# Kernel tuning notes

Measured on AMD Instinct MI355X. Metric: run time of the kernel, lower is better.

## Reference

```python
import jax, jax.numpy as jnp
import numpy as np

HEAD_COUNT = 6  # module scales by head_count**-0.5, not head_size
SCALE = HEAD_COUNT ** (-0.5)


def setup_inputs() -> dict:
    key = jax.random.key(0)
    kx, kq, kk, kv = jax.random.split(key, 4)
    B, T, C, H = 512, 128, 384, 64
    x = jax.random.normal(kx, (B, T, C), dtype=jnp.float32)
    init = (1.0 / np.sqrt(C)).astype(np.float32)
    Wq = jax.random.normal(kq, (C, H), dtype=jnp.float32) * init
    Wk = jax.random.normal(kk, (C, H), dtype=jnp.float32) * init
    Wv = jax.random.normal(kv, (C, H), dtype=jnp.float32) * init
    return {"x": x, "Wq": Wq, "Wk": Wk, "Wv": Wv}


def reference(x, Wq, Wk, Wv):
    # x: [B, T, C]; Wq/Wk/Wv: [C, H]
    q = jnp.einsum('btc,ch->bth', x, Wq)
    k = jnp.einsum('btc,ch->bth', x, Wk)
    v = jnp.einsum('btc,ch->bth', x, Wv)
    # scores: [B, T, T], scaled by head_count**-0.5 (faithful to source)
    scores = jnp.einsum('bth,bsh->bts', q, k) * SCALE
    T = x.shape[1]
    causal = jnp.tril(jnp.ones((T, T), dtype=bool))
    scores = jnp.where(causal, scores, -jnp.inf)
    weights = jax.nn.softmax(scores, axis=-1)
    # dropout omitted (eval mode / identity for reference baseline)
    return jnp.einsum('bts,bsh->bth', weights, v)
```

## Files before the change

### kernel.cpp

```cpp
#include <hip/hip_runtime.h>
#include <hip/hip_bf16.h>


#define B_ 512
#define T_ 128
#define C_ 384
#define H_ 64

typedef __bf16 bf16;
typedef __attribute__((ext_vector_type(8))) __bf16 bf16x8;
typedef __attribute__((ext_vector_type(4))) __bf16 bf16x4;
typedef __attribute__((ext_vector_type(4))) float f32x4;


__launch_bounds__(256, 2)
__global__ void head_fused(const float* __restrict__ x,
                           const float* __restrict__ Wq,
                           const float* __restrict__ Wk,
                           const float* __restrict__ Wv,
                           float* __restrict__ out)
{
    __shared__ bf16 lds[32256];
    bf16* Ws  = lds;
    bf16* Qs  = lds + 7680;
    bf16* Ks  = lds + 15872;
    bf16* Vts = lds + 24064;
    bf16* Ps  = lds + 7680;

    const int tid  = threadIdx.x;
    const int w    = tid >> 6;
    const int lane = tid & 63;
    const int lm   = lane & 15;
    const int quad = lane >> 4;
    const int b    = blockIdx.x;

    const float* xb = x + (size_t)b * (T_ * C_);

    f32x4 acc[2][12];
#pragma unroll
    for (int i = 0; i < 2; ++i)
#pragma unroll
        for (int t = 0; t < 12; ++t) acc[i][t] = (f32x4){0.f, 0.f, 0.f, 0.f};

    for (int kc = 0; kc < 12; ++kc) {
#pragma unroll
        for (int it = 0; it < 6; ++it) {
            int u   = tid + it * 256;
            int h   = u & 63;
            int rem = u >> 6;
            int j   = rem >> 3;
            int k4  = rem & 7;
            const float* Wp = (j == 0) ? Wq : (j == 1) ? Wk : Wv;
            const float* g  = Wp + (kc * 32 + k4 * 4) * H_ + h;
            float f0 = g[0], f1 = g[64], f2 = g[128], f3 = g[192];
            bf16x4 v4 = {(bf16)f0, (bf16)f1, (bf16)f2, (bf16)f3};
            *(bf16x4*)&Ws[(j * 64 + h) * 40 + k4 * 4] = v4;
        }
        __syncthreads();

        bf16x8 afr[2];
#pragma unroll
        for (int i = 0; i < 2; ++i) {
            const float4* xp =
                (const float4*)(xb + (32 * w + 16 * i + lm) * C_ + kc * 32 + quad * 8);
            float4 p0 = xp[0], p1 = xp[1];
            afr[i] = (bf16x8){(bf16)p0.x, (bf16)p0.y, (bf16)p0.z, (bf16)p0.w,
                              (bf16)p1.x, (bf16)p1.y, (bf16)p1.z, (bf16)p1.w};
        }
#pragma unroll
        for (int tn = 0; tn < 12; ++tn) {
            bf16x8 bfr = *(const bf16x8*)&Ws[(16 * tn + lm) * 40 + quad * 8];
            acc[0][tn] = __builtin_amdgcn_mfma_f32_16x16x32_bf16(afr[0], bfr, acc[0][tn], 0, 0, 0);
            acc[1][tn] = __builtin_amdgcn_mfma_f32_16x16x32_bf16(afr[1], bfr, acc[1][tn], 0, 0, 0);
        }
        __syncthreads();
    }

#pragma unroll
    for (int i = 0; i < 2; ++i) {
#pragma unroll
        for (int tn = 0; tn < 12; ++tn) {
            int gn = 16 * tn + lm;
            int j = gn >> 6, h = gn & 63;
            int m0 = 32 * w + 16 * i + quad * 4;
            if (j == 2) {
                bf16x4 v4 = {(bf16)acc[i][tn][0], (bf16)acc[i][tn][1],
                             (bf16)acc[i][tn][2], (bf16)acc[i][tn][3]};
                int pc = (m0 & 7) | ((((m0 >> 3) ^ (h & 15)) & 15) << 3);
                *(bf16x4*)&Vts[h * 128 + pc] = v4;
            } else {
                bf16* dst = (j == 0) ? Qs : Ks;
#pragma unroll
                for (int r = 0; r < 4; ++r) {
                    int m = m0 + r;
                    int pc = (h & 7) | ((((h >> 3) ^ (m & 7)) & 7) << 3);
                    dst[m * 64 + pc] = (bf16)acc[i][tn][r];
                }
            }
        }
    }
    __syncthreads();

    const float SCALE = 0.40824829046386307f;
    const int tmg0 = w, tmg1 = 7 - w;

    f32x4 sacc[2][8];
#pragma unroll
    for (int i = 0; i < 2; ++i)
#pragma unroll
        for (int t = 0; t < 8; ++t) sacc[i][t] = (f32x4){0.f, 0.f, 0.f, 0.f};

#pragma unroll
    for (int i = 0; i < 2; ++i) {
        const int tm = i ? tmg1 : tmg0;
        const int mrow = 16 * tm + lm;
        bf16x8 qa[2];
#pragma unroll
        for (int ks = 0; ks < 2; ++ks) {
            int phys = ((ks * 4 + quad) ^ (mrow & 7)) & 7;
            qa[ks] = *(const bf16x8*)&Qs[mrow * 64 + phys * 8];
        }
#pragma unroll
        for (int tn = 0; tn < 8; ++tn) {
            if (tn <= tm) {
                int nrow = 16 * tn + lm;
#pragma unroll
                for (int ks = 0; ks < 2; ++ks) {
                    int phys = ((ks * 4 + quad) ^ (nrow & 7)) & 7;
                    bf16x8 kb = *(const bf16x8*)&Ks[nrow * 64 + phys * 8];
                    sacc[i][tn] =
                        __builtin_amdgcn_mfma_f32_16x16x32_bf16(qa[ks], kb, sacc[i][tn], 0, 0, 0);
                }
            }
        }
    }

#pragma unroll
    for (int i = 0; i < 2; ++i) {
        const int tm = i ? tmg1 : tmg0;
#pragma unroll
        for (int r = 0; r < 4; ++r) {
            int m = 16 * tm + quad * 4 + r;
            float mx = -1e30f;
#pragma unroll
            for (int tn = 0; tn < 8; ++tn) {
                if (tn <= tm) {
                    int n = 16 * tn + lm;
                    float v = (n <= m) ? sacc[i][tn][r] * SCALE : -1e30f;
                    sacc[i][tn][r] = v;
                    mx = fmaxf(mx, v);
                }
            }
#pragma unroll
            for (int off = 1; off < 16; off <<= 1) mx = fmaxf(mx, __shfl_xor(mx, off, 16));
            float sum = 0.f;
#pragma unroll
            for (int tn = 0; tn < 8; ++tn) {
                if (tn <= tm) {
                    float e = __expf(sacc[i][tn][r] - mx);
                    sacc[i][tn][r] = e;
                    sum += e;
                }
            }
#pragma unroll
            for (int off = 1; off < 16; off <<= 1) sum += __shfl_xor(sum, off, 16);
            float inv = 1.f / sum;
#pragma unroll
            for (int tn = 0; tn < 8; ++tn) {
                if (tn <= tm) sacc[i][tn][r] *= inv;
            }
        }
    }

    __syncthreads();

#pragma unroll
    for (int i = 0; i < 2; ++i) {
        const int tm = i ? tmg1 : tmg0;
#pragma unroll
        for (int tn = 0; tn < 8; ++tn) {
            if (tn <= tm) {
                int n = 16 * tn + lm;
#pragma unroll
                for (int r = 0; r < 4; ++r) {
                    int m = 16 * tm + quad * 4 + r;
                    int pc = (n & 7) | ((((n >> 3) ^ (m & 15)) & 15) << 3);
                    Ps[m * 128 + pc] = (bf16)sacc[i][tn][r];
                }
            }
        }
        if ((tm & 1) == 0) {
            int m = 16 * tm + lm;
            int c0 = 16 * (tm + 1) + quad * 4;
            int pc = (c0 & 7) | ((((c0 >> 3) ^ (m & 15)) & 15) << 3);
            *(bf16x4*)&Ps[m * 128 + pc] =
                (bf16x4){(bf16)0.f, (bf16)0.f, (bf16)0.f, (bf16)0.f};
        }
    }

    f32x4 oacc[2][4];
#pragma unroll
    for (int i = 0; i < 2; ++i)
#pragma unroll
        for (int t = 0; t < 4; ++t) oacc[i][t] = (f32x4){0.f, 0.f, 0.f, 0.f};

#pragma unroll
    for (int i = 0; i < 2; ++i) {
        const int tm = i ? tmg1 : tmg0;
        const int mrow = 16 * tm + lm;
        const int nks = (tm + 2) >> 1;
        for (int ks = 0; ks < nks; ++ks) {
            int unit = ks * 4 + quad;
            int phys = (unit ^ (mrow & 15)) & 15;
            bf16x8 pa = *(const bf16x8*)&Ps[mrow * 128 + phys * 8];
#pragma unroll
            for (int th = 0; th < 4; ++th) {
                int hrow = 16 * th + lm;
                int ph2 = (unit ^ (hrow & 15)) & 15;
                bf16x8 vb = *(const bf16x8*)&Vts[hrow * 128 + ph2 * 8];
                oacc[i][th] =
                    __builtin_amdgcn_mfma_f32_16x16x32_bf16(pa, vb, oacc[i][th], 0, 0, 0);
            }
        }
    }

    float* ob = out + (size_t)b * (T_ * H_);
#pragma unroll
    for (int i = 0; i < 2; ++i) {
        const int tm = i ? tmg1 : tmg0;
#pragma unroll
        for (int th = 0; th < 4; ++th) {
            int h = 16 * th + lm;
#pragma unroll
            for (int r = 0; r < 4; ++r) {
                int m = 16 * tm + quad * 4 + r;
                ob[m * 64 + h] = oacc[i][th][r];
            }
        }
    }
}

extern "C" void kernel_launch(void* const* d_in, const int* in_sizes, int n_in,
                              void* d_out, int out_size, void* d_ws, size_t ws_size,
                              hipStream_t stream) {
    const float* x  = (const float*)d_in[0];
    const float* Wq = (const float*)d_in[1];
    const float* Wk = (const float*)d_in[2];
    const float* Wv = (const float*)d_in[3];
    float* o = (float*)d_out;
    head_fused<<<dim3(B_), dim3(256), 0, stream>>>(x, Wq, Wk, Wv, o);
}
```

Measured before the change: 173.6 us.

## Pre-convert weights to bf16 in a separate kernel and use 512-thread blocks

A small pre-pass kernel transposes and converts Wq/Wk/Wv to a bf16 [192x384] buffer in workspace. The main kernel then reads weight fragments straight from global/L2 instead of staging them in LDS each k-chunk, which removes the per-chunk __syncthreads pairs and shrinks LDS use. Blocks grow to 512 threads (8 waves), each owning one 16-row tile, which drops the previous balanced causal pairing of row tiles. The cost is an extra launch, more global weight traffic per block, and uneven causal work across waves.

Result: slower. 217.4 us (+25.2%).

```diff
diff --git a/kernel.cpp b/kernel.cpp
--- a/kernel.cpp
+++ b/kernel.cpp
@@ -12,20 +12,32 @@
 typedef __attribute__((ext_vector_type(4))) __bf16 bf16x4;
 typedef __attribute__((ext_vector_type(4))) float f32x4;
 
-
-__launch_bounds__(256, 2)
+__global__ void wt_conv(const float* __restrict__ Wq,
+                        const float* __restrict__ Wk,
+                        const float* __restrict__ Wv,
+                        bf16* __restrict__ Wt)
+{
+    int idx = blockIdx.x * 256 + threadIdx.x;
+    int n  = idx / 48;
+    int k0 = (idx - n * 48) * 8;
+    int j = n >> 6, h = n & 63;
+    const float* W = (j == 0) ? Wq : (j == 1) ? Wk : Wv;
+    bf16x8 v;
+#pragma unroll
+    for (int r = 0; r < 8; ++r) v[r] = (bf16)W[(k0 + r) * 64 + h];
+    *(bf16x8*)&Wt[n * 384 + k0] = v;
+}
+
+__launch_bounds__(512, 4)
 __global__ void head_fused(const float* __restrict__ x,
-                           const float* __restrict__ Wq,
-                           const float* __restrict__ Wk,
-                           const float* __restrict__ Wv,
+                           const bf16* __restrict__ Wt,
                            float* __restrict__ out)
 {
-    __shared__ bf16 lds[32256];
-    bf16* Ws  = lds;
-    bf16* Qs  = lds + 7680;
-    bf16* Ks  = lds + 15872;
-    bf16* Vts = lds + 24064;
-    bf16* Ps  = lds + 7680;
+    __shared__ bf16 lds[24576];
+    bf16* Qs  = lds;
+    bf16* Ks  = lds + 8192;
+    bf16* Vts = lds + 16384;
+    bf16* Ps  = lds;
 
     const int tid  = threadIdx.x;
     const int w    = tid >> 6;
@@ -35,207 +47,152 @@
     const int b    = blockIdx.x;
 
     const float* xb = x + (size_t)b * (T_ * C_);
-
-    f32x4 acc[2][12];
-#pragma unroll
-    for (int i = 0; i < 2; ++i)
-#pragma unroll
-        for (int t = 0; t < 12; ++t) acc[i][t] = (f32x4){0.f, 0.f, 0.f, 0.f};
-
+    const int mrow = 16 * w + lm;
+
+    f32x4 acc[12];
+#pragma unroll
+    for (int t = 0; t < 12; ++t) acc[t] = (f32x4){0.f, 0.f, 0.f, 0.f};
+
+#pragma unroll 1
     for (int kc = 0; kc < 12; ++kc) {
-#pragma unroll
-        for (int it = 0; it < 6; ++it) {
-            int u   = tid + it * 256;
-            int h   = u & 63;
-            int rem = u >> 6;
-            int j   = rem >> 3;
-            int k4  = rem & 7;
-            const float* Wp = (j == 0) ? Wq : (j == 1) ? Wk : Wv;
-            const float* g  = Wp + (kc * 32 + k4 * 4) * H_ + h;
-            float f0 = g[0], f1 = g[64], f2 = g[128], f3 = g[192];
-            bf16x4 v4 = {(bf16)f0, (bf16)f1, (bf16)f2, (bf16)f3};
-            *(bf16x4*)&Ws[(j * 64 + h) * 40 + k4 * 4] = v4;
-        }
-        __syncthreads();
-
-        bf16x8 afr[2];
-#pragma unroll
-        for (int i = 0; i < 2; ++i) {
-            const float4* xp =
-                (const float4*)(xb + (32 * w + 16 * i + lm) * C_ + kc * 32 + quad * 8);
-            float4 p0 = xp[0], p1 = xp[1];
-            afr[i] = (bf16x8){(bf16)p0.x, (bf16)p0.y, (bf16)p0.z, (bf16)p0.w,
-                              (bf16)p1.x, (bf16)p1.y, (bf16)p1.z, (bf16)p1.w};
-        }
+        const float4* xp = (const float4*)(xb + mrow * C_ + kc * 32 + quad * 8);
+        float4 p0 = xp[0], p1 = xp[1];
+        bf16x8 afr = {(bf16)p0.x, (bf16)p0.y, (bf16)p0.z, (bf16)p0.w,
+                      (bf16)p1.x, (bf16)p1.y, (bf16)p1.z, (bf16)p1.w};
 #pragma unroll
         for (int tn = 0; tn < 12; ++tn) {
-            bf16x8 bfr = *(const bf16x8*)&Ws[(16 * tn + lm) * 40 + quad * 8];
-            acc[0][tn] = __builtin_amdgcn_mfma_f32_16x16x32_bf16(afr[0], bfr, acc[0][tn], 0, 0, 0);
-            acc[1][tn] = __builtin_amdgcn_mfma_f32_16x16x32_bf16(afr[1], bfr, acc[1][tn], 0, 0, 0);
-        }
-        __syncthreads();
-    }
-
-#pragma unroll
-    for (int i = 0; i < 2; ++i) {
-#pragma unroll
-        for (int tn = 0; tn < 12; ++tn) {
-            int gn = 16 * tn + lm;
-            int j = gn >> 6, h = gn & 63;
-            int m0 = 32 * w + 16 * i + quad * 4;
-            if (j == 2) {
-                bf16x4 v4 = {(bf16)acc[i][tn][0], (bf16)acc[i][tn][1],
-                             (bf16)acc[i][tn][2], (bf16)acc[i][tn][3]};
-                int pc = (m0 & 7) | ((((m0 >> 3) ^ (h & 15)) & 15) << 3);
-                *(bf16x4*)&Vts[h * 128 + pc] = v4;
-            } else {
-                bf16* dst = (j == 0) ? Qs : Ks;
-#pragma unroll
-                for (int r = 0; r < 4; ++r) {
-                    int m = m0 + r;
-                    int pc = (h & 7) | ((((h >> 3) ^ (m & 7)) & 7) << 3);
-                    dst[m * 64 + pc] = (bf16)acc[i][tn][r];
-                }
+            bf16x8 bfr = *(const bf16x8*)&Wt[(16 * tn + lm) * 384 + kc * 32 + quad * 8];
+            acc[tn] = __builtin_amdgcn_mfma_f32_16x16x32_bf16(afr, bfr, acc[tn], 0, 0, 0);
+        }
+    }
+
+#pragma unroll
+    for (int tn = 0; tn < 12; ++tn) {
+        int h  = (16 * tn + lm) & 63;
+        int m0 = 16 * w + quad * 4;
+        if (tn >= 8) {
+            bf16x4 v4 = {(bf16)acc[tn][0], (bf16)acc[tn][1],
+                         (bf16)acc[tn][2], (bf16)acc[tn][3]};
+            int pc = (m0 & 7) | ((((m0 >> 3) ^ (h & 15)) & 15) << 3);
+            *(bf16x4*)&Vts[h * 128 + pc] = v4;
+        } else {
+            bf16* dst = (tn < 4) ? Qs : Ks;
+#pragma unroll
+            for (int r = 0; r < 4; ++r) {
+                int m = m0 + r;
+                int pc = (h & 7) | ((((h >> 3) ^ (m & 7)) & 7) << 3);
+                dst[m * 64 + pc] = (bf16)acc[tn][r];
             }
         }
     }
     __syncthreads();
 
     const float SCALE = 0.40824829046386307f;
-    const int tmg0 = w, tmg1 = 7 - w;
-
-    f32x4 sacc[2][8];
-#pragma unroll
-    for (int i = 0; i < 2; ++i)
-#pragma unroll
-        for (int t = 0; t < 8; ++t) sacc[i][t] = (f32x4){0.f, 0.f, 0.f, 0.f};
-
-#pragma unroll
-    for (int i = 0; i < 2; ++i) {
-        const int tm = i ? tmg1 : tmg0;
-        const int mrow = 16 * tm + lm;
-        bf16x8 qa[2];
-#pragma unroll
-        for (int ks = 0; ks < 2; ++ks) {
-            int phys = ((ks * 4 + quad) ^ (mrow & 7)) & 7;
-            qa[ks] = *(const bf16x8*)&Qs[mrow * 64 + phys * 8];
-        }
-#pragma unroll
-        for (int tn = 0; tn < 8; ++tn) {
-            if (tn <= tm) {
-                int nrow = 16 * tn + lm;
-#pragma unroll
-                for (int ks = 0; ks < 2; ++ks) {
-                    int phys = ((ks * 4 + quad) ^ (nrow & 7)) & 7;
-                    bf16x8 kb = *(const bf16x8*)&Ks[nrow * 64 + phys * 8];
-                    sacc[i][tn] =
-                        __builtin_amdgcn_mfma_f32_16x16x32_bf16(qa[ks], kb, sacc[i][tn], 0, 0, 0);
-                }
-            }
-        }
-    }
-
-#pragma unroll
-    for (int i = 0; i < 2; ++i) {
-        const int tm = i ? tmg1 : tmg0;
-#pragma unroll
-        for (int r = 0; r < 4; ++r) {
-            int m = 16 * tm + quad * 4 + r;
-            float mx = -1e30f;
-#pragma unroll
-            for (int tn = 0; tn < 8; ++tn) {
-                if (tn <= tm) {
-                    int n = 16 * tn + lm;
-                    float v = (n <= m) ? sacc[i][tn][r] * SCALE : -1e30f;
-                    sacc[i][tn][r] = v;
-                    mx = fmaxf(mx, v);
-                }
-            }
-#pragma unroll
-            for (int off = 1; off < 16; off <<= 1) mx = fmaxf(mx, __shfl_xor(mx, off, 16));
-            float sum = 0.f;
-#pragma unroll
-            for (int tn = 0; tn < 8; ++tn) {
-                if (tn <= tm) {
-                    float e = __expf(sacc[i][tn][r] - mx);
-                    sacc[i][tn][r] = e;
-                    sum += e;
-                }
-            }
-#pragma unroll
-            for (int off = 1; off < 16; off <<= 1) sum += __shfl_xor(sum, off, 16);
-            float inv = 1.f / sum;
-#pragma unroll
-            for (int tn = 0; tn < 8; ++tn) {
-                if (tn <= tm) sacc[i][tn][r] *= inv;
-            }
-        }
-    }
-
-    __syncthreads();
-
-#pragma unroll
-    for (int i = 0; i < 2; ++i) {
-        const int tm = i ? tmg1 : tmg0;
+    const int tm = w;
+
+    f32x4 sacc[8];
+#pragma unroll
+    for (int t = 0; t < 8; ++t) sacc[t] = (f32x4){0.f, 0.f, 0.f, 0.f};
+
+    bf16x8 qa[2];
+#pragma unroll
+    for (int ks = 0; ks < 2; ++ks) {
+        int phys = ((ks * 4 + quad) ^ (mrow & 7)) & 7;
+        qa[ks] = *(const bf16x8*)&Qs[mrow * 64 + phys * 8];
+    }
+#pragma unroll
+    for (int tn = 0; tn < 8; ++tn) {
+        if (tn <= tm) {
+            int nrow = 16 * tn + lm;
+#pragma unroll
+            for (int ks = 0; ks < 2; ++ks) {
+                int phys = ((ks * 4 + quad) ^ (nrow & 7)) & 7;
+                bf16x8 kb = *(const bf16x8*)&Ks[nrow * 64 + phys * 8];
+                sacc[tn] = __builtin_amdgcn_mfma_f32_16x16x32_bf16(qa[ks], kb, sacc[tn], 0, 0, 0);
+            }
+        }
+    }
+
+#pragma unroll
+    for (int r = 0; r < 4; ++r) {
+        int m = 16 * tm + quad * 4 + r;
+        float mx = -1e30f;
 #pragma unroll
         for (int tn = 0; tn < 8; ++tn) {
             if (tn <= tm) {
                 int n = 16 * tn + lm;
-#pragma unroll
-                for (int r = 0; r < 4; ++r) {
-                    int m = 16 * tm + quad * 4 + r;
-                    int pc = (n & 7) | ((((n >> 3) ^ (m & 15)) & 15) << 3);
-                    Ps[m * 128 + pc] = (bf16)sacc[i][tn][r];
-                }
-            }
-        }
-        if ((tm & 1) == 0) {
-            int m = 16 * tm + lm;
-            int c0 = 16 * (tm + 1) + quad * 4;
-            int pc = (c0 & 7) | ((((c0 >> 3) ^ (m & 15)) & 15) << 3);
-            *(bf16x4*)&Ps[m * 128 + pc] =
-                (bf16x4){(bf16)0.f, (bf16)0.f, (bf16)0.f, (bf16)0.f};
-        }
-    }
-
-    f32x4 oacc[2][4];
-#pragma unroll
-    for (int i = 0; i < 2; ++i)
-#pragma unroll
-        for (int t = 0; t < 4; ++t) oacc[i][t] = (f32x4){0.f, 0.f, 0.f, 0.f};
-
-#pragma unroll
-    for (int i = 0; i < 2; ++i) {
-        const int tm = i ? tmg1 : tmg0;
-        const int mrow = 16 * tm + lm;
-        const int nks = (tm + 2) >> 1;
-        for (int ks = 0; ks < nks; ++ks) {
-            int unit = ks * 4 + quad;
-            int phys = (unit ^ (mrow & 15)) & 15;
-            bf16x8 pa = *(const bf16x8*)&Ps[mrow * 128 + phys * 8];
-#pragma unroll
-            for (int th = 0; th < 4; ++th) {
-                int hrow = 16 * th + lm;
-                int ph2 = (unit ^ (hrow & 15)) & 15;
-                bf16x8 vb = *(const bf16x8*)&Vts[hrow * 128 + ph2 * 8];
-                oacc[i][th] =
-                    __builtin_amdgcn_mfma_f32_16x16x32_bf16(pa, vb, oacc[i][th], 0, 0, 0);
-            }
-        }
-    }
-
-    float* ob = out + (size_t)b * (T_ * H_);
-#pragma unroll
-    for (int i = 0; i < 2; ++i) {
-        const int tm = i ? tmg1 : tmg0;
-#pragma unroll
-        for (int th = 0; th < 4; ++th) {
-            int h = 16 * th + lm;
+                float v = (n <= m) ? sacc[tn][r] * SCALE : -1e30f;
+                sacc[tn][r] = v;
+                mx = fmaxf(mx, v);
+            }
+        }
+#pragma unroll
+        for (int off = 1; off < 16; off <<= 1) mx = fmaxf(mx, __shfl_xor(mx, off, 16));
+        float sum = 0.f;
+#pragma unroll
+        for (int tn = 0; tn < 8; ++tn) {
+            if (tn <= tm) {
+                float e = __expf(sacc[tn][r] - mx);
+                sacc[tn][r] = e;
+                sum += e;
+            }
+        }
+#pragma unroll
+        for (int off = 1; off < 16; off <<= 1) sum += __shfl_xor(sum, off, 16);
+        float inv = 1.f / sum;
+#pragma unroll
+        for (int tn = 0; tn < 8; ++tn) {
+            if (tn <= tm) sacc[tn][r] *= inv;
+        }
+    }
+
+    __syncthreads();
+
+#pragma unroll
+    for (int tn = 0; tn < 8; ++tn) {
+        if (tn <= tm) {
+            int n = 16 * tn + lm;
 #pragma unroll
             for (int r = 0; r < 4; ++r) {
                 int m = 16 * tm + quad * 4 + r;
-                ob[m * 64 + h] = oacc[i][th][r];
-            }
+                int pc = (n & 7) | ((((n >> 3) ^ (m & 15)) & 15) << 3);
+                Ps[m * 128 + pc] = (bf16)sacc[tn][r];
+            }
+        }
+    }
+    if ((tm & 1) == 0) {
+        int m = 16 * tm + lm;
+        int c0 = 16 * (tm + 1) + quad * 4;
+        int pc = (c0 & 7) | ((((c0 >> 3) ^ (m & 15)) & 15) << 3);
+        *(bf16x4*)&Ps[m * 128 + pc] = (bf16x4){(bf16)0.f, (bf16)0.f, (bf16)0.f, (bf16)0.f};
+    }
+
+    f32x4 oacc[4];
+#pragma unroll
+    for (int t = 0; t < 4; ++t) oacc[t] = (f32x4){0.f, 0.f, 0.f, 0.f};
+
+    const int nks = (tm + 2) >> 1;
+    for (int ks = 0; ks < nks; ++ks) {
+        int unit = ks * 4 + quad;
+        int phys = (unit ^ (mrow & 15)) & 15;
+        bf16x8 pa = *(const bf16x8*)&Ps[mrow * 128 + phys * 8];
+#pragma unroll
+        for (int th = 0; th < 4; ++th) {
+            int hrow = 16 * th + lm;
+            int ph2 = (unit ^ (hrow & 15)) & 15;
+            bf16x8 vb = *(const bf16x8*)&Vts[hrow * 128 + ph2 * 8];
+            oacc[th] = __builtin_amdgcn_mfma_f32_16x16x32_bf16(pa, vb, oacc[th], 0, 0, 0);
+        }
+    }
+
+    float* ob = out + (size_t)b * (T_ * H_);
+#pragma unroll
+    for (int th = 0; th < 4; ++th) {
+        int h = 16 * th + lm;
+#pragma unroll
+        for (int r = 0; r < 4; ++r) {
+            int m = 16 * tm + quad * 4 + r;
+            ob[m * 64 + h] = oacc[th][r];
         }
     }
 }
@@ -247,6 +204,8 @@
     const float* Wq = (const float*)d_in[1];
     const float* Wk = (const float*)d_in[2];
     const float* Wv = (const float*)d_in[3];
-    float* o = (float*)d_out;
-    head_fused<<<dim3(B_), dim3(256), 0, stream>>>(x, Wq, Wk, Wv, o);
+    float* o  = (float*)d_out;
+    bf16* Wt  = (bf16*)d_ws;
+    wt_conv<<<dim3(36), dim3(256), 0, stream>>>(Wq, Wk, Wv, Wt);
+    head_fused<<<dim3(B_), dim3(512), 0, stream>>>(x, Wt, o);
 }
```

## Pre-convert weights to transposed bf16 in workspace and read fragments from global

Applied to the files above, without the earlier changes.

Adds a small pre-kernel that converts Wq/Wk/Wv to a transposed bf16 matrix in the workspace. The main kernel then reads MFMA B-fragments straight from global/L2 instead of staging weights through LDS, which removes two barriers per k-chunk and shrinks LDS use. It also double-buffers the x loads one chunk ahead in registers. The costs are an extra kernel launch and repeated per-block global reads of the weights, which rely on L2 hits.

Result: slower. 191.9 us (+10.5%).

```diff
diff --git a/kernel.cpp b/kernel.cpp
--- a/kernel.cpp
+++ b/kernel.cpp
@@ -12,20 +12,32 @@
 typedef __attribute__((ext_vector_type(4))) __bf16 bf16x4;
 typedef __attribute__((ext_vector_type(4))) float f32x4;
 
+__global__ void wt_conv(const float* __restrict__ Wq,
+                        const float* __restrict__ Wk,
+                        const float* __restrict__ Wv,
+                        bf16* __restrict__ Wt)
+{
+    int idx = blockIdx.x * 256 + threadIdx.x;
+    int n  = idx / 48;
+    int k0 = (idx - n * 48) * 8;
+    int j = n >> 6, h = n & 63;
+    const float* W = (j == 0) ? Wq : (j == 1) ? Wk : Wv;
+    bf16x8 v;
+#pragma unroll
+    for (int r = 0; r < 8; ++r) v[r] = (bf16)W[(k0 + r) * 64 + h];
+    *(bf16x8*)&Wt[n * 384 + k0] = v;
+}
 
 __launch_bounds__(256, 2)
 __global__ void head_fused(const float* __restrict__ x,
-                           const float* __restrict__ Wq,
-                           const float* __restrict__ Wk,
-                           const float* __restrict__ Wv,
+                           const bf16* __restrict__ Wt,
                            float* __restrict__ out)
 {
-    __shared__ bf16 lds[32256];
-    bf16* Ws  = lds;
-    bf16* Qs  = lds + 7680;
-    bf16* Ks  = lds + 15872;
-    bf16* Vts = lds + 24064;
-    bf16* Ps  = lds + 7680;
+    __shared__ bf16 lds[24576];
+    bf16* Qs  = lds;
+    bf16* Ks  = lds + 8192;
+    bf16* Vts = lds + 16384;
+    bf16* Ps  = lds;
 
     const int tid  = threadIdx.x;
     const int w    = tid >> 6;
@@ -42,54 +54,54 @@
 #pragma unroll
         for (int t = 0; t < 12; ++t) acc[i][t] = (f32x4){0.f, 0.f, 0.f, 0.f};
 
+    const float* xr0 = xb + (32 * w + lm) * C_ + quad * 8;
+    const float* xr1 = xb + (32 * w + 16 + lm) * C_ + quad * 8;
+
+    float4 xbuf[2][2][2];
+    xbuf[0][0][0] = ((const float4*)xr0)[0];
+    xbuf[0][0][1] = ((const float4*)xr0)[1];
+    xbuf[0][1][0] = ((const float4*)xr1)[0];
+    xbuf[0][1][1] = ((const float4*)xr1)[1];
+
+#pragma unroll 2
     for (int kc = 0; kc < 12; ++kc) {
-#pragma unroll
-        for (int it = 0; it < 6; ++it) {
-            int u   = tid + it * 256;
-            int h   = u & 63;
-            int rem = u >> 6;
-            int j   = rem >> 3;
-            int k4  = rem & 7;
-            const float* Wp = (j == 0) ? Wq : (j == 1) ? Wk : Wv;
-            const float* g  = Wp + (kc * 32 + k4 * 4) * H_ + h;
-            float f0 = g[0], f1 = g[64], f2 = g[128], f3 = g[192];
-            bf16x4 v4 = {(bf16)f0, (bf16)f1, (bf16)f2, (bf16)f3};
-            *(bf16x4*)&Ws[(j * 64 + h) * 40 + k4 * 4] = v4;
-        }
-        __syncthreads();
-
+        const int cb = kc & 1;
+        if (kc < 11) {
+            const float4* n0 = (const float4*)(xr0 + (kc + 1) * 32);
+            const float4* n1 = (const float4*)(xr1 + (kc + 1) * 32);
+            xbuf[cb ^ 1][0][0] = n0[0];
+            xbuf[cb ^ 1][0][1] = n0[1];
+            xbuf[cb ^ 1][1][0] = n1[0];
+            xbuf[cb ^ 1][1][1] = n1[1];
+        }
         bf16x8 afr[2];
 #pragma unroll
         for (int i = 0; i < 2; ++i) {
-            const float4* xp =
-                (const float4*)(xb + (32 * w + 16 * i + lm) * C_ + kc * 32 + quad * 8);
-            float4 p0 = xp[0], p1 = xp[1];
+            float4 p0 = xbuf[cb][i][0], p1 = xbuf[cb][i][1];
             afr[i] = (bf16x8){(bf16)p0.x, (bf16)p0.y, (bf16)p0.z, (bf16)p0.w,
                               (bf16)p1.x, (bf16)p1.y, (bf16)p1.z, (bf16)p1.w};
         }
 #pragma unroll
         for (int tn = 0; tn < 12; ++tn) {
-            bf16x8 bfr = *(const bf16x8*)&Ws[(16 * tn + lm) * 40 + quad * 8];
+            bf16x8 bfr = *(const bf16x8*)&Wt[(16 * tn + lm) * 384 + kc * 32 + quad * 8];
             acc[0][tn] = __builtin_amdgcn_mfma_f32_16x16x32_bf16(afr[0], bfr, acc[0][tn], 0, 0, 0);
             acc[1][tn] = __builtin_amdgcn_mfma_f32_16x16x32_bf16(afr[1], bfr, acc[1][tn], 0, 0, 0);
         }
-        __syncthreads();
     }
 
 #pragma unroll
     for (int i = 0; i < 2; ++i) {
 #pragma unroll
         for (int tn = 0; tn < 12; ++tn) {
-            int gn = 16 * tn + lm;
-            int j = gn >> 6, h = gn & 63;
+            int h  = (16 * tn + lm) & 63;
             int m0 = 32 * w + 16 * i + quad * 4;
-            if (j == 2) {
+            if (tn >= 8) {
                 bf16x4 v4 = {(bf16)acc[i][tn][0], (bf16)acc[i][tn][1],
                              (bf16)acc[i][tn][2], (bf16)acc[i][tn][3]};
                 int pc = (m0 & 7) | ((((m0 >> 3) ^ (h & 15)) & 15) << 3);
                 *(bf16x4*)&Vts[h * 128 + pc] = v4;
             } else {
-                bf16* dst = (j == 0) ? Qs : Ks;
+                bf16* dst = (tn < 4) ? Qs : Ks;
 #pragma unroll
                 for (int r = 0; r < 4; ++r) {
                     int m = m0 + r;
@@ -113,12 +125,12 @@
 #pragma unroll
     for (int i = 0; i < 2; ++i) {
         const int tm = i ? tmg1 : tmg0;
-        const int mrow = 16 * tm + lm;
+        const int mr = 16 * tm + lm;
         bf16x8 qa[2];
 #pragma unroll
         for (int ks = 0; ks < 2; ++ks) {
-            int phys = ((ks * 4 + quad) ^ (mrow & 7)) & 7;
-            qa[ks] = *(const bf16x8*)&Qs[mrow * 64 + phys * 8];
+            int phys = ((ks * 4 + quad) ^ (mr & 7)) & 7;
+            qa[ks] = *(const bf16x8*)&Qs[mr * 64 + phys * 8];
         }
 #pragma unroll
         for (int tn = 0; tn < 8; ++tn) {
@@ -193,8 +205,7 @@
             int m = 16 * tm + lm;
             int c0 = 16 * (tm + 1) + quad * 4;
             int pc = (c0 & 7) | ((((c0 >> 3) ^ (m & 15)) & 15) << 3);
-            *(bf16x4*)&Ps[m * 128 + pc] =
-                (bf16x4){(bf16)0.f, (bf16)0.f, (bf16)0.f, (bf16)0.f};
+            *(bf16x4*)&Ps[m * 128 + pc] = (bf16x4){(bf16)0.f, (bf16)0.f, (bf16)0.f, (bf16)0.f};
         }
     }
 
@@ -207,12 +218,12 @@
 #pragma unroll
     for (int i = 0; i < 2; ++i) {
         const int tm = i ? tmg1 : tmg0;
-        const int mrow = 16 * tm + lm;
+        const int mr = 16 * tm + lm;
         const int nks = (tm + 2) >> 1;
         for (int ks = 0; ks < nks; ++ks) {
             int unit = ks * 4 + quad;
-            int phys = (unit ^ (mrow & 15)) & 15;
-            bf16x8 pa = *(const bf16x8*)&Ps[mrow * 128 + phys * 8];
+            int phys = (unit ^ (mr & 15)) & 15;
+            bf16x8 pa = *(const bf16x8*)&Ps[mr * 128 + phys * 8];
 #pragma unroll
             for (int th = 0; th < 4; ++th) {
                 int hrow = 16 * th + lm;
@@ -248,5 +259,7 @@
     const float* Wk = (const float*)d_in[2];
     const float* Wv = (const float*)d_in[3];
     float* o = (float*)d_out;
-    head_fused<<<dim3(B_), dim3(256), 0, stream>>>(x, Wq, Wk, Wv, o);
+    bf16* Wt = (bf16*)d_ws;
+    wt_conv<<<dim3(36), dim3(256), 0, stream>>>(Wq, Wk, Wv, Wt);
+    head_fused<<<dim3(B_), dim3(256), 0, stream>>>(x, Wt, o);
 }
```
